# Kernel optimization log

Hardware: AMD Instinct MI355X
Metric: run time of the kernel (lower is better)

## Reference

```python
import jax, jax.numpy as jnp
import numpy as np

N = 50000
E = 800000
IN_C = 64
OUT_C = 128
T = 4


def setup_inputs() -> dict:
    key = jax.random.key(0)
    ks = jax.random.split(key, 12)
    s = 0.05
    return {
        "x": jax.random.normal(ks[0], (N, IN_C), dtype=jnp.float32),
        "u": jax.random.normal(ks[1], (N, OUT_C), dtype=jnp.float32),
        "edge_index": jax.random.randint(ks[2], (2, E), 0, N, dtype=jnp.int32),
        # w1: Linear(in_channels, out_channels)
        "w1_W": jax.random.normal(ks[3], (OUT_C, IN_C), dtype=jnp.float32) * s,
        "w1_b": jnp.zeros((OUT_C,), dtype=jnp.float32),
        # sigmod MLP: three Linear(out, out) layers
        "m1_W": jax.random.normal(ks[4], (OUT_C, OUT_C), dtype=jnp.float32) * s,
        "m1_b": jnp.zeros((OUT_C,), dtype=jnp.float32),
        "m2_W": jax.random.normal(ks[5], (OUT_C, OUT_C), dtype=jnp.float32) * s,
        "m2_b": jnp.zeros((OUT_C,), dtype=jnp.float32),
        "m3_W": jax.random.normal(ks[6], (OUT_C, OUT_C), dtype=jnp.float32) * s,
        "m3_b": jnp.zeros((OUT_C,), dtype=jnp.float32),
        # w2: Linear(out, out) for graph readout
        "w2_W": jax.random.normal(ks[7], (OUT_C, OUT_C), dtype=jnp.float32) * s,
        "w2_b": jnp.zeros((OUT_C,), dtype=jnp.float32),
    }


def reference(x, u, edge_index, w1_W, w1_b, m1_W, m1_b, m2_W, m2_b, m3_W, m3_b, w2_W, w2_b):
    n_nodes = x.shape[0]
    src = edge_index[0]  # gather source (u_j)
    dst = edge_index[1]  # scatter-add target
    xw = x @ w1_W.T + w1_b  # [N, out]; identical every iteration
    for _ in range(T):
        agg = jax.ops.segment_sum(u[src], dst, num_segments=n_nodes)  # [N, out]
        h = jax.nn.relu(agg @ m1_W.T + m1_b)
        h = jax.nn.relu(h @ m2_W.T + m2_b)
        h = jnp.tanh(h @ m3_W.T + m3_b)
        u = jax.nn.relu(xw + h)
    g = jnp.sum(u, axis=0, keepdims=True)  # e @ u with e = ones [1, N]
    return g @ w2_W.T + w2_b  # [1, out]
```

## Files before the change

### kernel.cpp

```cpp
#include <hip/hip_runtime.h>
#include <hip/hip_bf16.h>

#define NN 50000
#define NE 800000
#define CI 64
#define CO 128
#define SCANB 49
#define NB 196
#define CHUNK 2048
#define NCH 391

typedef __attribute__((ext_vector_type(8))) short bf16x8;
typedef __attribute__((ext_vector_type(4))) float f32x4;

__device__ __forceinline__ unsigned short f2bf(float f) {
  unsigned int u = __float_as_uint(f);
  u += 0x7fffu + ((u >> 16) & 1u);
  return (unsigned short)(u >> 16);
}
__device__ __forceinline__ float bf2f_lo(unsigned int p) { return __uint_as_float(p << 16); }
__device__ __forceinline__ float bf2f_hi(unsigned int p) { return __uint_as_float(p & 0xffff0000u); }
__device__ __forceinline__ unsigned int pk2(float lo, float hi) {
  return ((unsigned int)f2bf(hi) << 16) | (unsigned int)f2bf(lo);
}

__global__ __launch_bounds__(256) void k_bhist(const int* __restrict__ dst,
                                               int* __restrict__ bcnt) {
  __shared__ int lc[NB];
  int tid = threadIdx.x;
  for (int t = tid; t < NB; t += 256) lc[t] = 0;
  __syncthreads();
  int base = blockIdx.x * CHUNK;
#pragma unroll
  for (int i = 0; i < 8; ++i) {
    int idx = base + i * 256 + tid;
    if (idx < NE) atomicAdd(&lc[dst[idx] >> 8], 1);
  }
  __syncthreads();
  for (int t = tid; t < NB; t += 256) if (lc[t]) atomicAdd(&bcnt[t], lc[t]);
}

__global__ __launch_bounds__(256) void k_bscan(const int* __restrict__ bcnt,
                                               int* __restrict__ bkt_off,
                                               int* __restrict__ bkt_cur) {
  __shared__ int s[256];
  int t = threadIdx.x;
  int v = (t < NB) ? bcnt[t] : 0;
  s[t] = v;
  __syncthreads();
  for (int off = 1; off < 256; off <<= 1) {
    int x = (t >= off) ? s[t - off] : 0;
    __syncthreads();
    s[t] += x;
    __syncthreads();
  }
  if (t < NB) { int e = s[t] - v; bkt_off[t] = e; bkt_cur[t] = e; }
  if (t == 0) bkt_off[NB] = NE;
}

__global__ __launch_bounds__(256) void k_bin(const int* __restrict__ src,
                                             const int* __restrict__ dst,
                                             int* __restrict__ bkt_cur,
                                             uint2* __restrict__ pairs) {
  __shared__ int lcnt[NB];
  __shared__ int lbase[NB];
  int tid = threadIdx.x;
  for (int t = tid; t < NB; t += 256) lcnt[t] = 0;
  __syncthreads();
  int base = blockIdx.x * CHUNK;
  int ds[8], sr[8], rk[8];
#pragma unroll
  for (int i = 0; i < 8; ++i) {
    int idx = base + i * 256 + tid;
    if (idx < NE) {
      ds[i] = dst[idx]; sr[i] = src[idx];
      rk[i] = atomicAdd(&lcnt[ds[i] >> 8], 1);
    } else ds[i] = -1;
  }
  __syncthreads();
  for (int t = tid; t < NB; t += 256)
    lbase[t] = lcnt[t] ? atomicAdd(&bkt_cur[t], lcnt[t]) : 0;
  __syncthreads();
#pragma unroll
  for (int i = 0; i < 8; ++i) {
    if (ds[i] >= 0) {
      uint2 pr; pr.x = (unsigned)sr[i]; pr.y = (unsigned)ds[i];
      pairs[lbase[ds[i] >> 8] + rk[i]] = pr;
    }
  }
}

__global__ __launch_bounds__(256) void k_deg(const uint2* __restrict__ pairs,
                                             const int* __restrict__ bkt_off,
                                             int* __restrict__ deg) {
  __shared__ int lc[256];
  int t = threadIdx.x, b = blockIdx.x;
  lc[t] = 0;
  __syncthreads();
  int beg = bkt_off[b], end = bkt_off[b + 1];
  for (int i = beg + t; i < end; i += 256)
    atomicAdd(&lc[pairs[i].y & 255], 1);
  __syncthreads();
  int node = (b << 8) + t;
  if (node < NN) deg[node] = lc[t];
}

__global__ __launch_bounds__(256) void k_scan1(const int* __restrict__ deg, int* __restrict__ bsum) {
  int i0 = blockIdx.x * 1024 + threadIdx.x * 4;
  int s = 0;
#pragma unroll
  for (int j = 0; j < 4; ++j) { int i = i0 + j; if (i < NN) s += deg[i]; }
#pragma unroll
  for (int off = 32; off; off >>= 1) s += __shfl_down(s, off);
  __shared__ int ws[4];
  if ((threadIdx.x & 63) == 0) ws[threadIdx.x >> 6] = s;
  __syncthreads();
  if (threadIdx.x == 0) bsum[blockIdx.x] = ws[0] + ws[1] + ws[2] + ws[3];
}

__global__ __launch_bounds__(64) void k_scan2(const int* __restrict__ bsum, int* __restrict__ boff) {
  int t = threadIdx.x;
  int v = (t < SCANB) ? bsum[t] : 0;
  int incl = v;
#pragma unroll
  for (int off = 1; off < 64; off <<= 1) {
    int o = __shfl_up(incl, off);
    if (t >= off) incl += o;
  }
  if (t < SCANB) boff[t] = incl - v;
}

__global__ __launch_bounds__(256) void k_scan3(const int* __restrict__ deg, const int* __restrict__ boff,
                                               int* __restrict__ row_off) {
  int b = blockIdx.x;
  int i0 = b * 1024 + threadIdx.x * 4;
  int v[4]; int tsum = 0;
#pragma unroll
  for (int j = 0; j < 4; ++j) { int i = i0 + j; v[j] = (i < NN) ? deg[i] : 0; tsum += v[j]; }
  int incl = tsum;
#pragma unroll
  for (int off = 1; off < 64; off <<= 1) {
    int o = __shfl_up(incl, off);
    if ((threadIdx.x & 63) >= (unsigned)off) incl += o;
  }
  __shared__ int ws[4];
  int w = threadIdx.x >> 6;
  if ((threadIdx.x & 63) == 63) ws[w] = incl;
  __syncthreads();
  int wbase = 0;
  for (int k = 0; k < 4; ++k) if (k < w) wbase += ws[k];
  int excl = boff[b] + wbase + incl - tsum;
#pragma unroll
  for (int j = 0; j < 4; ++j) { int i = i0 + j; if (i < NN) row_off[i] = excl; excl += v[j]; }
  if (b == 0 && threadIdx.x == 0) row_off[NN] = NE;
}

__global__ __launch_bounds__(256) void k_fillB(const uint2* __restrict__ pairs,
                                               const int* __restrict__ bkt_off,
                                               const int* __restrict__ row_off,
                                               int* __restrict__ ssrc) {
  __shared__ int lcur[256];
  int t = threadIdx.x, b = blockIdx.x;
  lcur[t] = 0;
  __syncthreads();
  int beg = bkt_off[b], end = bkt_off[b + 1];
  for (int i = beg + t; i < end; i += 256) {
    uint2 e = pairs[i];
    int d = (int)e.y;
    int pos = row_off[d] + atomicAdd(&lcur[d & 255], 1);
    ssrc[pos] = (int)e.x;
  }
}

__global__ void k_cvt_w(const float* __restrict__ w1, const float* __restrict__ m1,
                        const float* __restrict__ m2, const float* __restrict__ m3,
                        unsigned short* __restrict__ o) {
  int i = blockIdx.x * blockDim.x + threadIdx.x;
  if (i >= 57344) return;
  float v;
  if (i < 8192) v = w1[i];
  else if (i < 24576) v = m1[i - 8192];
  else if (i < 40960) v = m2[i - 24576];
  else v = m3[i - 40960];
  o[i] = f2bf(v);
}

__global__ void k_cvt4(const float* __restrict__ in, unsigned short* __restrict__ out, int n4) {
  int i = blockIdx.x * blockDim.x + threadIdx.x;
  if (i >= n4) return;
  float4 v = *(const float4*)(in + i * 4);
  ushort2 lo = { f2bf(v.x), f2bf(v.y) };
  ushort2 hi = { f2bf(v.z), f2bf(v.w) };
  *(ushort2*)(out + i * 4) = lo;
  *(ushort2*)(out + i * 4 + 2) = hi;
}

__global__ __launch_bounds__(256) void k_gather(const int* __restrict__ row_off,
    const int* __restrict__ ssrc, const unsigned short* __restrict__ ubf,
    unsigned short* __restrict__ agg) {
  int wave = threadIdx.x >> 6, lane = threadIdx.x & 63;
  int g = lane >> 4, c = lane & 15;
  int node = blockIdx.x * 16 + wave * 4 + g;
  int gl = g << 4;
  int beg = row_off[node], end = row_off[node + 1];
  float a[8];
#pragma unroll
  for (int i = 0; i < 8; ++i) a[i] = 0.f;

#define ADD8(r) { a[0] += bf2f_lo(r.x); a[1] += bf2f_hi(r.x); \
                  a[2] += bf2f_lo(r.y); a[3] += bf2f_hi(r.y); \
                  a[4] += bf2f_lo(r.z); a[5] += bf2f_hi(r.z); \
                  a[6] += bf2f_lo(r.w); a[7] += bf2f_hi(r.w); }

  for (int base = beg; base < end; base += 16) {
    int e = base + c;
    int sid = (e < end) ? ssrc[e] : 0;
    int cnt = min(16, end - base);
    int j = 0;
    for (; j + 4 <= cnt; j += 4) {
      int s0 = __shfl(sid, gl + j + 0);
      int s1 = __shfl(sid, gl + j + 1);
      int s2 = __shfl(sid, gl + j + 2);
      int s3 = __shfl(sid, gl + j + 3);
      uint4 r0 = *(const uint4*)(ubf + (size_t)s0 * CO + c * 8);
      uint4 r1 = *(const uint4*)(ubf + (size_t)s1 * CO + c * 8);
      uint4 r2 = *(const uint4*)(ubf + (size_t)s2 * CO + c * 8);
      uint4 r3 = *(const uint4*)(ubf + (size_t)s3 * CO + c * 8);
      ADD8(r0); ADD8(r1); ADD8(r2); ADD8(r3);
    }
    for (; j < cnt; ++j) {
      int s = __shfl(sid, gl + j);
      uint4 r = *(const uint4*)(ubf + (size_t)s * CO + c * 8);
      ADD8(r);
    }
  }
#undef ADD8
  uint4 o;
  o.x = pk2(a[0], a[1]); o.y = pk2(a[2], a[3]);
  o.z = pk2(a[4], a[5]); o.w = pk2(a[6], a[7]);
  *(uint4*)(agg + (size_t)node * CO + c * 8) = o;
}

__global__ __launch_bounds__(256) void k_xw(const unsigned short* __restrict__ A,
    const unsigned short* __restrict__ W, const float* __restrict__ bias,
    unsigned short* __restrict__ xwb) {
  int wave = threadIdx.x >> 6, lane = threadIdx.x & 63;
  int m = lane & 15, q = lane >> 4;
  int row0 = blockIdx.x * 64 + wave * 16;
  int arow = row0 + m; if (arow >= NN) arow = NN - 1;
  const unsigned short* Ar = A + (size_t)arow * CI;
  f32x4 acc[8];
#pragma unroll
  for (int tt = 0; tt < 8; ++tt) acc[tt] = (f32x4){0.f, 0.f, 0.f, 0.f};
#pragma unroll
  for (int ks = 0; ks < CI; ks += 32) {
    bf16x8 a = *(const bf16x8*)(Ar + ks + q * 8);
#pragma unroll
    for (int tt = 0; tt < 8; ++tt) {
      bf16x8 b = *(const bf16x8*)(W + (size_t)(tt * 16 + m) * CI + ks + q * 8);
      acc[tt] = __builtin_amdgcn_mfma_f32_16x16x32_bf16(a, b, acc[tt], 0, 0, 0);
    }
  }
#pragma unroll
  for (int tt = 0; tt < 8; ++tt) {
    int o = tt * 16 + m;
    float bv = bias[o];
#pragma unroll
    for (int r = 0; r < 4; ++r) {
      int node = row0 + q * 4 + r;
      if (node < NN) xwb[(size_t)node * CO + o] = f2bf(acc[tt][r] + bv);
    }
  }
}

__global__ __launch_bounds__(512, 4) void k_mlp(const unsigned short* __restrict__ agg,
    const unsigned short* __restrict__ W1, const unsigned short* __restrict__ W2,
    const unsigned short* __restrict__ W3,
    const float* __restrict__ b1, const float* __restrict__ b2, const float* __restrict__ b3,
    const unsigned short* __restrict__ xwb, unsigned short* __restrict__ uout) {
  constexpr int SP = 136;
  __shared__ unsigned short lds[16384 + 8 * 16 * SP];
  unsigned short* wt = lds;
  int tid = threadIdx.x;
  int wave = tid >> 6, lane = tid & 63;
  int m = lane & 15, q = lane >> 4;
  int row0 = blockIdx.x * 128 + wave * 16;
  unsigned short* L = lds + 16384 + wave * 16 * SP;
  int ar = row0 + m; if (ar >= NN) ar = NN - 1;
  const unsigned short* Ap = agg + (size_t)ar * CO;

  uint4 wreg[4];
  const int trb = (tid >> 4) & 7;
  const int tc  = tid & 15;
  const int ldst0 = (tid >> 4) * 128 + ((tc ^ trb) << 3);
  auto stage_load = [&](const unsigned short* W) {
#pragma unroll
    for (int j = 0; j < 4; ++j)
      wreg[j] = *(const uint4*)(W + ((j * 512 + tid) << 3));
  };
  auto stage_write = [&]() {
#pragma unroll
    for (int j = 0; j < 4; ++j)
      *(uint4*)(wt + ldst0 + j * 4096) = wreg[j];
  };
  auto bfrag = [&](int t, int ks) -> bf16x8 {
    int ch = (ks >> 3) + q;
    return *(const bf16x8*)(wt + (t * 16 + m) * 128 + ((ch ^ (m & 7)) << 3));
  };

  stage_load(W1);
  bf16x8 ar4[4];
#pragma unroll
  for (int k4 = 0; k4 < 4; ++k4) ar4[k4] = *(const bf16x8*)(Ap + k4 * 32 + q * 8);
  stage_write();

  f32x4 acc[8];
#pragma unroll
  for (int t = 0; t < 8; ++t) acc[t] = (f32x4){0.f, 0.f, 0.f, 0.f};
  __syncthreads();

#pragma unroll
  for (int k4 = 0; k4 < 4; ++k4) {
#pragma unroll
    for (int t = 0; t < 8; ++t) {
      bf16x8 b = bfrag(t, k4 * 32);
      acc[t] = __builtin_amdgcn_mfma_f32_16x16x32_bf16(ar4[k4], b, acc[t], 0, 0, 0);
    }
  }
  stage_load(W2);
#pragma unroll
  for (int t = 0; t < 8; ++t) {
    float bv = b1[t * 16 + m];
#pragma unroll
    for (int r = 0; r < 4; ++r)
      L[(q * 4 + r) * SP + t * 16 + m] = f2bf(fmaxf(acc[t][r] + bv, 0.f));
  }
  __syncthreads();
  stage_write();
#pragma unroll
  for (int t = 0; t < 8; ++t) acc[t] = (f32x4){0.f, 0.f, 0.f, 0.f};
  __syncthreads();

#pragma unroll
  for (int ks = 0; ks < CO; ks += 32) {
    bf16x8 a = *(const bf16x8*)(L + m * SP + ks + q * 8);
#pragma unroll
    for (int t = 0; t < 8; ++t) {
      bf16x8 b = bfrag(t, ks);
      acc[t] = __builtin_amdgcn_mfma_f32_16x16x32_bf16(a, b, acc[t], 0, 0, 0);
    }
  }
  stage_load(W3);
#pragma unroll
  for (int t = 0; t < 8; ++t) {
    float bv = b2[t * 16 + m];
#pragma unroll
    for (int r = 0; r < 4; ++r)
      L[(q * 4 + r) * SP + t * 16 + m] = f2bf(fmaxf(acc[t][r] + bv, 0.f));
  }
  __syncthreads();
  stage_write();
#pragma unroll
  for (int t = 0; t < 8; ++t) acc[t] = (f32x4){0.f, 0.f, 0.f, 0.f};
  __syncthreads();

#pragma unroll
  for (int ks = 0; ks < CO; ks += 32) {
    bf16x8 a = *(const bf16x8*)(L + m * SP + ks + q * 8);
#pragma unroll
    for (int t = 0; t < 8; ++t) {
      bf16x8 b = bfrag(t, ks);
      acc[t] = __builtin_amdgcn_mfma_f32_16x16x32_bf16(a, b, acc[t], 0, 0, 0);
    }
  }
#pragma unroll
  for (int t = 0; t < 8; ++t) {
    float bv = b3[t * 16 + m];
#pragma unroll
    for (int r = 0; r < 4; ++r) {
      float v = acc[t][r] + bv;
      float e = __expf(2.f * v);
      v = 1.f - 2.f / (e + 1.f);
      L[(q * 4 + r) * SP + t * 16 + m] = f2bf(v);
    }
  }
  int ln = lane >> 2, lc = lane & 3;
  int gnode = row0 + ln;
  if (gnode < NN) {
    const unsigned short* xr = xwb + (size_t)gnode * CO;
    unsigned short* ur = uout + (size_t)gnode * CO;
#pragma unroll
    for (int rnd = 0; rnd < 4; ++rnd) {
      int ch = (rnd * 4 + lc) * 8;
      uint4 h = *(const uint4*)(L + ln * SP + ch);
      uint4 xv = *(const uint4*)(xr + ch);
      uint4 o;
      o.x = pk2(fmaxf(bf2f_lo(h.x) + bf2f_lo(xv.x), 0.f), fmaxf(bf2f_hi(h.x) + bf2f_hi(xv.x), 0.f));
      o.y = pk2(fmaxf(bf2f_lo(h.y) + bf2f_lo(xv.y), 0.f), fmaxf(bf2f_hi(h.y) + bf2f_hi(xv.y), 0.f));
      o.z = pk2(fmaxf(bf2f_lo(h.z) + bf2f_lo(xv.z), 0.f), fmaxf(bf2f_hi(h.z) + bf2f_hi(xv.z), 0.f));
      o.w = pk2(fmaxf(bf2f_lo(h.w) + bf2f_lo(xv.w), 0.f), fmaxf(bf2f_hi(h.w) + bf2f_hi(xv.w), 0.f));
      *(uint4*)(ur + ch) = o;
    }
  }
}

__global__ __launch_bounds__(256) void k_reduce(const unsigned short* __restrict__ u,
                                                float* __restrict__ g) {
  int ch2 = threadIdx.x & 63;
  int sub = threadIdx.x >> 6;
  float a0 = 0.f, a1 = 0.f;
  for (int n = blockIdx.x * 4 + sub; n < NN; n += gridDim.x * 4) {
    unsigned int p = *(const unsigned int*)(u + (size_t)n * CO + ch2 * 2);
    a0 += bf2f_lo(p); a1 += bf2f_hi(p);
  }
  __shared__ float s0[256], s1[256];
  s0[threadIdx.x] = a0; s1[threadIdx.x] = a1;
  __syncthreads();
  if (sub == 0) {
    a0 = s0[ch2] + s0[64 + ch2] + s0[128 + ch2] + s0[192 + ch2];
    a1 = s1[ch2] + s1[64 + ch2] + s1[128 + ch2] + s1[192 + ch2];
    atomicAdd(&g[ch2 * 2], a0);
    atomicAdd(&g[ch2 * 2 + 1], a1);
  }
}

__global__ void k_final(const float* __restrict__ g, const float* __restrict__ w2,
                        const float* __restrict__ b2, float* __restrict__ outp) {
  __shared__ float sg[128];
  if (threadIdx.x < 128) sg[threadIdx.x] = g[threadIdx.x];
  __syncthreads();
  int j = threadIdx.x;
  if (j < 128) {
    float acc = b2[j];
    for (int c = 0; c < 128; ++c) acc += sg[c] * w2[j * 128 + c];
    outp[j] = acc;
  }
}

extern "C" void kernel_launch(void* const* d_in, const int* in_sizes, int n_in,
                              void* d_out, int out_size, void* d_ws, size_t ws_size,
                              hipStream_t stream) {
  (void)in_sizes; (void)n_in; (void)out_size; (void)ws_size;
  const float* x   = (const float*)d_in[0];
  const float* u0  = (const float*)d_in[1];
  const int*   ei  = (const int*)d_in[2];
  const float* w1W = (const float*)d_in[3];
  const float* w1b = (const float*)d_in[4];
  const float* m1W = (const float*)d_in[5];
  const float* m1b = (const float*)d_in[6];
  const float* m2W = (const float*)d_in[7];
  const float* m2b = (const float*)d_in[8];
  const float* m3W = (const float*)d_in[9];
  const float* m3b = (const float*)d_in[10];
  const float* w2W = (const float*)d_in[11];
  const float* w2b = (const float*)d_in[12];
  const int* esrc = ei;
  const int* edst = ei + NE;

  char* p = (char*)d_ws;
  auto carve = [&](size_t bytes) { char* r = p; p += (bytes + 255) & ~(size_t)255; return r; };
  unsigned short* xwb     = (unsigned short*)carve((size_t)NN * CO * 2);
  unsigned short* ubf     = (unsigned short*)carve((size_t)NN * CO * 2);
  unsigned short* agg     = (unsigned short*)carve((size_t)NN * CO * 2);
  unsigned short* xb      = (unsigned short*)carve((size_t)NN * CI * 2);
  unsigned short* wbf     = (unsigned short*)carve((size_t)57344 * 2);
  int*            row_off = (int*)carve((size_t)(NN + 1) * 4);
  int*            deg     = (int*)carve((size_t)NN * 4);
  int*            ssrc    = (int*)carve((size_t)NE * 4);
  uint2*          pairs   = (uint2*)carve((size_t)NE * 8);
  int*            bkt_cnt = (int*)carve((size_t)NB * 4);
  int*            bkt_off = (int*)carve((size_t)(NB + 1) * 4);
  int*            bkt_cur = (int*)carve((size_t)NB * 4);
  int*            bsum    = (int*)carve((size_t)SCANB * 4);
  int*            boff    = (int*)carve((size_t)SCANB * 4);
  float*          g       = (float*)carve(128 * 4);

  hipMemsetAsync(bkt_cnt, 0, (size_t)NB * 4, stream);
  hipMemsetAsync(g, 0, 128 * 4, stream);

  k_bhist<<<NCH, 256, 0, stream>>>(edst, bkt_cnt);
  k_bscan<<<1, 256, 0, stream>>>(bkt_cnt, bkt_off, bkt_cur);
  k_bin<<<NCH, 256, 0, stream>>>(esrc, edst, bkt_cur, pairs);
  k_deg<<<NB, 256, 0, stream>>>(pairs, bkt_off, deg);
  k_scan1<<<SCANB, 256, 0, stream>>>(deg, bsum);
  k_scan2<<<1, 64, 0, stream>>>(bsum, boff);
  k_scan3<<<SCANB, 256, 0, stream>>>(deg, boff, row_off);
  k_fillB<<<NB, 256, 0, stream>>>(pairs, bkt_off, row_off, ssrc);

  k_cvt_w<<<(57344 + 255) / 256, 256, 0, stream>>>(w1W, m1W, m2W, m3W, wbf);
  k_cvt4<<<(NN * CI / 4 + 255) / 256, 256, 0, stream>>>(x, xb, NN * CI / 4);
  k_cvt4<<<(NN * CO / 4 + 255) / 256, 256, 0, stream>>>(u0, ubf, NN * CO / 4);

  k_xw<<<(NN + 63) / 64, 256, 0, stream>>>(xb, wbf, w1b, xwb);

  const unsigned short* Wm1 = wbf + 8192;
  const unsigned short* Wm2 = wbf + 8192 + 16384;
  const unsigned short* Wm3 = wbf + 8192 + 2 * 16384;
  const int GM = (NN + 127) / 128;
  for (int it = 0; it < 4; ++it) {
    k_gather<<<NN / 16, 256, 0, stream>>>(row_off, ssrc, ubf, agg);
    k_mlp<<<GM, 512, 0, stream>>>(agg, Wm1, Wm2, Wm3, m1b, m2b, m3b, xwb, ubf);
  }

  k_reduce<<<256, 256, 0, stream>>>(ubf, g);
  k_final<<<1, 128, 0, stream>>>(g, w2W, w2b, (float*)d_out);
}
```

Before: 412.9 us.

## Fuse CSR degree/scan/fill into one bucket kernel and convert x inside xw

The degree count, three-stage prefix scan and CSR fill are merged into a single per-bucket kernel. Because nodes are already binned into contiguous 256-node buckets, each bucket's row offsets follow from the bucket's base offset plus a local shared-memory scan. Separately, the x-to-bf16 conversion kernel is removed and k_xw reads fp32 x directly, converting in registers. This drops four launches and the round trips through the deg and xb buffers, at the cost of a serial shared-memory scan with many barriers inside each block.

```diff
diff --git a/kernel.cpp b/kernel.cpp
--- a/kernel.cpp
+++ b/kernel.cpp
@@ -5,7 +5,6 @@
 #define NE 800000
 #define CI 64
 #define CO 128
-#define SCANB 49
 #define NB 196
 #define CHUNK 2048
 #define NCH 391
@@ -90,10 +89,12 @@
   }
 }
 
-__global__ __launch_bounds__(256) void k_deg(const uint2* __restrict__ pairs,
-                                             const int* __restrict__ bkt_off,
-                                             int* __restrict__ deg) {
+__global__ __launch_bounds__(256) void k_fillB(const uint2* __restrict__ pairs,
+                                               const int* __restrict__ bkt_off,
+                                               int* __restrict__ row_off,
+                                               int* __restrict__ ssrc) {
   __shared__ int lc[256];
+  __shared__ int ls[256];
   int t = threadIdx.x, b = blockIdx.x;
   lc[t] = 0;
   __syncthreads();
@@ -101,73 +102,24 @@
   for (int i = beg + t; i < end; i += 256)
     atomicAdd(&lc[pairs[i].y & 255], 1);
   __syncthreads();
+  int v = lc[t];
+  ls[t] = v;
+  __syncthreads();
+  for (int off = 1; off < 256; off <<= 1) {
+    int x = (t >= off) ? ls[t - off] : 0;
+    __syncthreads();
+    ls[t] += x;
+    __syncthreads();
+  }
+  int excl = ls[t] - v;
   int node = (b << 8) + t;
-  if (node < NN) deg[node] = lc[t];
-}
-
-__global__ __launch_bounds__(256) void k_scan1(const int* __restrict__ deg, int* __restrict__ bsum) {
-  int i0 = blockIdx.x * 1024 + threadIdx.x * 4;
-  int s = 0;
-#pragma unroll
-  for (int j = 0; j < 4; ++j) { int i = i0 + j; if (i < NN) s += deg[i]; }
-#pragma unroll
-  for (int off = 32; off; off >>= 1) s += __shfl_down(s, off);
-  __shared__ int ws[4];
-  if ((threadIdx.x & 63) == 0) ws[threadIdx.x >> 6] = s;
-  __syncthreads();
-  if (threadIdx.x == 0) bsum[blockIdx.x] = ws[0] + ws[1] + ws[2] + ws[3];
-}
-
-__global__ __launch_bounds__(64) void k_scan2(const int* __restrict__ bsum, int* __restrict__ boff) {
-  int t = threadIdx.x;
-  int v = (t < SCANB) ? bsum[t] : 0;
-  int incl = v;
-#pragma unroll
-  for (int off = 1; off < 64; off <<= 1) {
-    int o = __shfl_up(incl, off);
-    if (t >= off) incl += o;
-  }
-  if (t < SCANB) boff[t] = incl - v;
-}
-
-__global__ __launch_bounds__(256) void k_scan3(const int* __restrict__ deg, const int* __restrict__ boff,
-                                               int* __restrict__ row_off) {
-  int b = blockIdx.x;
-  int i0 = b * 1024 + threadIdx.x * 4;
-  int v[4]; int tsum = 0;
-#pragma unroll
-  for (int j = 0; j < 4; ++j) { int i = i0 + j; v[j] = (i < NN) ? deg[i] : 0; tsum += v[j]; }
-  int incl = tsum;
-#pragma unroll
-  for (int off = 1; off < 64; off <<= 1) {
-    int o = __shfl_up(incl, off);
-    if ((threadIdx.x & 63) >= (unsigned)off) incl += o;
-  }
-  __shared__ int ws[4];
-  int w = threadIdx.x >> 6;
-  if ((threadIdx.x & 63) == 63) ws[w] = incl;
-  __syncthreads();
-  int wbase = 0;
-  for (int k = 0; k < 4; ++k) if (k < w) wbase += ws[k];
-  int excl = boff[b] + wbase + incl - tsum;
-#pragma unroll
-  for (int j = 0; j < 4; ++j) { int i = i0 + j; if (i < NN) row_off[i] = excl; excl += v[j]; }
-  if (b == 0 && threadIdx.x == 0) row_off[NN] = NE;
-}
-
-__global__ __launch_bounds__(256) void k_fillB(const uint2* __restrict__ pairs,
-                                               const int* __restrict__ bkt_off,
-                                               const int* __restrict__ row_off,
-                                               int* __restrict__ ssrc) {
-  __shared__ int lcur[256];
-  int t = threadIdx.x, b = blockIdx.x;
-  lcur[t] = 0;
-  __syncthreads();
-  int beg = bkt_off[b], end = bkt_off[b + 1];
+  if (node < NN) row_off[node] = beg + excl;
+  if (b == 0 && t == 0) row_off[NN] = NE;
+  lc[t] = beg + excl;
+  __syncthreads();
   for (int i = beg + t; i < end; i += 256) {
     uint2 e = pairs[i];
-    int d = (int)e.y;
-    int pos = row_off[d] + atomicAdd(&lcur[d & 255], 1);
+    int pos = atomicAdd(&lc[e.y & 255], 1);
     ssrc[pos] = (int)e.x;
   }
 }
@@ -241,20 +193,25 @@
   *(uint4*)(agg + (size_t)node * CO + c * 8) = o;
 }
 
-__global__ __launch_bounds__(256) void k_xw(const unsigned short* __restrict__ A,
+__global__ __launch_bounds__(256) void k_xw(const float* __restrict__ X,
     const unsigned short* __restrict__ W, const float* __restrict__ bias,
     unsigned short* __restrict__ xwb) {
   int wave = threadIdx.x >> 6, lane = threadIdx.x & 63;
   int m = lane & 15, q = lane >> 4;
   int row0 = blockIdx.x * 64 + wave * 16;
   int arow = row0 + m; if (arow >= NN) arow = NN - 1;
-  const unsigned short* Ar = A + (size_t)arow * CI;
+  const float* Xr = X + (size_t)arow * CI;
   f32x4 acc[8];
 #pragma unroll
   for (int tt = 0; tt < 8; ++tt) acc[tt] = (f32x4){0.f, 0.f, 0.f, 0.f};
 #pragma unroll
   for (int ks = 0; ks < CI; ks += 32) {
-    bf16x8 a = *(const bf16x8*)(Ar + ks + q * 8);
+    float4 f0 = *(const float4*)(Xr + ks + q * 8);
+    float4 f1 = *(const float4*)(Xr + ks + q * 8 + 4);
+    union { unsigned int u[4]; bf16x8 v; } cv;
+    cv.u[0] = pk2(f0.x, f0.y); cv.u[1] = pk2(f0.z, f0.w);
+    cv.u[2] = pk2(f1.x, f1.y); cv.u[3] = pk2(f1.z, f1.w);
+    bf16x8 a = cv.v;
 #pragma unroll
     for (int tt = 0; tt < 8; ++tt) {
       bf16x8 b = *(const bf16x8*)(W + (size_t)(tt * 16 + m) * CI + ks + q * 8);
@@ -462,17 +419,13 @@
   unsigned short* xwb     = (unsigned short*)carve((size_t)NN * CO * 2);
   unsigned short* ubf     = (unsigned short*)carve((size_t)NN * CO * 2);
   unsigned short* agg     = (unsigned short*)carve((size_t)NN * CO * 2);
-  unsigned short* xb      = (unsigned short*)carve((size_t)NN * CI * 2);
   unsigned short* wbf     = (unsigned short*)carve((size_t)57344 * 2);
   int*            row_off = (int*)carve((size_t)(NN + 1) * 4);
-  int*            deg     = (int*)carve((size_t)NN * 4);
   int*            ssrc    = (int*)carve((size_t)NE * 4);
   uint2*          pairs   = (uint2*)carve((size_t)NE * 8);
   int*            bkt_cnt = (int*)carve((size_t)NB * 4);
   int*            bkt_off = (int*)carve((size_t)(NB + 1) * 4);
   int*            bkt_cur = (int*)carve((size_t)NB * 4);
-  int*            bsum    = (int*)carve((size_t)SCANB * 4);
-  int*            boff    = (int*)carve((size_t)SCANB * 4);
   float*          g       = (float*)carve(128 * 4);
 
   hipMemsetAsync(bkt_cnt, 0, (size_t)NB * 4, stream);
@@ -481,17 +434,12 @@
   k_bhist<<<NCH, 256, 0, stream>>>(edst, bkt_cnt);
   k_bscan<<<1, 256, 0, stream>>>(bkt_cnt, bkt_off, bkt_cur);
   k_bin<<<NCH, 256, 0, stream>>>(esrc, edst, bkt_cur, pairs);
-  k_deg<<<NB, 256, 0, stream>>>(pairs, bkt_off, deg);
-  k_scan1<<<SCANB, 256, 0, stream>>>(deg, bsum);
-  k_scan2<<<1, 64, 0, stream>>>(bsum, boff);
-  k_scan3<<<SCANB, 256, 0, stream>>>(deg, boff, row_off);
   k_fillB<<<NB, 256, 0, stream>>>(pairs, bkt_off, row_off, ssrc);
 
   k_cvt_w<<<(57344 + 255) / 256, 256, 0, stream>>>(w1W, m1W, m2W, m3W, wbf);
-  k_cvt4<<<(NN * CI / 4 + 255) / 256, 256, 0, stream>>>(x, xb, NN * CI / 4);
   k_cvt4<<<(NN * CO / 4 + 255) / 256, 256, 0, stream>>>(u0, ubf, NN * CO / 4);
 
-  k_xw<<<(NN + 63) / 64, 256, 0, stream>>>(xb, wbf, w1b, xwb);
+  k_xw<<<(NN + 63) / 64, 256, 0, stream>>>(x, wbf, w1b, xwb);
 
   const unsigned short* Wm1 = wbf + 8192;
   const unsigned short* Wm2 = wbf + 8192 + 16384;
```

Measured after the change: 400.2 us (median of 2 runs). 3.1% less time.
